# Optimization experiments

Hardware: AMD Instinct MI355X
Metric: run time of the kernel (lower is better)

The kernel has to match this reference:

```python
import jax, jax.numpy as jnp
import numpy as np

GROUPS = 8
EPS = 1e-5


def group_norm(x, gamma, beta):
    # x: (b, c, h, w); normalize per sample over each group of c//GROUPS channels and all spatial dims
    b, c, h, w = x.shape
    xg = x.reshape(b, GROUPS, c // GROUPS, h, w)
    mean = jnp.mean(xg, axis=(2, 3, 4), keepdims=True)
    var = jnp.var(xg, axis=(2, 3, 4), keepdims=True)
    xn = ((xg - mean) * jax.lax.rsqrt(var + EPS)).reshape(b, c, h, w)
    return xn * gamma[None, :, None, None] + beta[None, :, None, None]


def setup_inputs() -> dict:
    key = jax.random.key(0)
    k1, k2, k3 = jax.random.split(key, 3)
    b, c, h, w = 32, 256, 32, 32
    x = jax.random.normal(k1, (b, c, h, w), dtype=jnp.float32)
    qkv_w = jax.random.normal(k2, (3 * c, c), dtype=jnp.float32) * 0.02
    qkv_b = jnp.zeros((3 * c,), dtype=jnp.float32)
    out_w = jax.random.normal(k3, (c, c), dtype=jnp.float32) * 0.02
    out_b = jnp.zeros((c,), dtype=jnp.float32)
    gn_gamma = jnp.ones((c,), dtype=jnp.float32)
    gn_beta = jnp.zeros((c,), dtype=jnp.float32)
    return {"x": x, "gn_gamma": gn_gamma, "gn_beta": gn_beta,
            "qkv_w": qkv_w, "qkv_b": qkv_b, "out_w": out_w, "out_b": out_b}


def reference(x, gn_gamma, gn_beta, qkv_w, qkv_b, out_w, out_b):
    b, c, h, w = x.shape
    xn = group_norm(x, gn_gamma, gn_beta)
    # 1x1 conv == per-pixel linear: (b,c,h,w) x (3c,c) -> (b,3c,h,w)
    qkv = jnp.einsum('bchw,dc->bdhw', xn, qkv_w) + qkv_b[None, :, None, None]
    q, k, v = jnp.split(qkv, 3, axis=1)
    # (b, c, h, w) -> (b, hw, c)
    def tok(t):
        return t.transpose(0, 2, 3, 1).reshape(b, h * w, c)
    q, k, v = tok(q), tok(k), tok(v)
    scale = 1.0 / jnp.sqrt(jnp.asarray(c, dtype=x.dtype))
    scores = jnp.einsum('bnc,bmc->bnm', q, k) * scale  # (b, hw, hw)
    attn = jax.nn.softmax(scores, axis=-1)
    out = jnp.einsum('bnm,bmc->bnc', attn, v)  # (b, hw, c)
    out = out.reshape(b, h, w, c).transpose(0, 3, 1, 2)  # (b, c, h, w)
    out = jnp.einsum('bchw,dc->bdhw', out, out_w) + out_b[None, :, None, None]
    return out + x
```

## Files before the change

### kernel.cpp

```cpp
#include <hip/hip_runtime.h>
#include <hip/hip_bf16.h>
#include <stdint.h>


typedef __bf16 bf16_t;
typedef __bf16 bf16x4 __attribute__((ext_vector_type(4)));
typedef __bf16 bf16x8 __attribute__((ext_vector_type(8)));
typedef float f32x4 __attribute__((ext_vector_type(4)));
typedef float f32x16 __attribute__((ext_vector_type(16)));
typedef _Float16 f16x4 __attribute__((ext_vector_type(4)));

#define MFMA16(a, b, c) __builtin_amdgcn_mfma_f32_16x16x32_bf16((a), (b), (c), 0, 0, 0)
#define MFMA32(a, b, c) __builtin_amdgcn_mfma_f32_32x32x16_bf16((a), (b), (c), 0, 0, 0)
#define GLL16(g, l)                                                                     \
    __builtin_amdgcn_global_load_lds((const __attribute__((address_space(1))) void*)(g), \
                                     (__attribute__((address_space(3))) void*)(l), 16, 0, 0)

__global__ void cast_bf16(const float* __restrict__ s, bf16_t* __restrict__ d, int n) {
    for (int i = blockIdx.x * blockDim.x + threadIdx.x; i < n; i += gridDim.x * blockDim.x)
        d[i] = (bf16_t)s[i];
}

__global__ __launch_bounds__(256) void gn_kernel(const float* __restrict__ x,
                                                 const float* __restrict__ gamma,
                                                 const float* __restrict__ beta,
                                                 bf16_t* __restrict__ xn) {
    extern __shared__ char gsm[];
    float* red = (float*)(gsm + 65536);
    int bg = blockIdx.x, b = bg >> 3, g = bg & 7;
    const float* base = x + (size_t)(b * 256 + g * 32) * 1024;
    int tid = threadIdx.x;

    float s = 0.f, ss = 0.f;
    #pragma unroll 4
    for (int c = 0; c < 32; c++) {
        float4 v = *(const float4*)(base + c * 1024 + tid * 4);
        s += v.x + v.y + v.z + v.w;
        ss += v.x * v.x + v.y * v.y + v.z * v.z + v.w * v.w;
        f16x4 h = {(_Float16)v.x, (_Float16)v.y, (_Float16)v.z, (_Float16)v.w};
        *(f16x4*)(gsm + c * 2048 + ((tid * 8) ^ ((c & 7) << 4))) = h;
    }
    for (int off = 32; off; off >>= 1) { s += __shfl_down(s, off); ss += __shfl_down(ss, off); }
    if ((tid & 63) == 0) { red[tid >> 6] = s; red[4 + (tid >> 6)] = ss; }
    __syncthreads();
    float S = red[0] + red[1] + red[2] + red[3];
    float SS = red[4] + red[5] + red[6] + red[7];
    float mean = S * (1.0f / 32768.0f);
    float var = SS * (1.0f / 32768.0f) - mean * mean;
    float rstd = rsqrtf(var + 1e-5f);

    int c = tid & 31;
    float gam = gamma[g * 32 + c] * rstd;
    float bet = beta[g * 32 + c] - mean * gam;
    bf16_t* dst = xn + (size_t)(b * 1024) * 256 + g * 32 + c;
    #pragma unroll 4
    for (int it = 0; it < 128; it++) {
        int p = it * 8 + (tid >> 5);
        _Float16 hv = *(_Float16*)(gsm + c * 2048 + ((p * 2) ^ ((c & 7) << 4)));
        dst[(size_t)p * 256] = (bf16_t)((float)hv * gam + bet);
    }
}

__global__ __launch_bounds__(256) void gemm_qkv(const bf16_t* __restrict__ xn,
                                                const bf16_t* __restrict__ wq,
                                                const float* __restrict__ qkv_b,
                                                bf16_t* __restrict__ qb,
                                                bf16_t* __restrict__ kb,
                                                bf16_t* __restrict__ vt) {
    __shared__ char smem[65536];
    char* As = smem;
    char* Bs = smem + 32768;
    int tid = threadIdx.x;
    int m0 = blockIdx.x * 64, n0 = blockIdx.y * 64;
    const char* asrc = (const char*)xn + (size_t)m0 * 512;
    const char* bsrc = (const char*)wq + (size_t)n0 * 512;

    float4 ta[8], tb[8];
    #pragma unroll
    for (int i = 0; i < 8; i++) {
        int t = i * 256 + tid, row = t >> 5, sl = t & 31;
        ta[i] = *(const float4*)(asrc + row * 512 + sl * 16);
        tb[i] = *(const float4*)(bsrc + row * 512 + sl * 16);
    }
    #pragma unroll
    for (int i = 0; i < 8; i++) {
        int t = i * 256 + tid, row = t >> 5, sl = t & 31;
        int off = (sl * 16) ^ ((row & 7) << 4);
        *(float4*)(As + row * 512 + off) = ta[i];
        *(float4*)(Bs + row * 512 + off) = tb[i];
    }
    __syncthreads();

    int wv = tid >> 6, lane = tid & 63, lrow = lane & 15, lgr = lane >> 4;
    int arow = wv * 16 + lrow;
    f32x4 acc[4] = {};
    #pragma unroll
    for (int s = 0; s < 8; s++) {
        int koff = s * 64 + lgr * 16;
        bf16x8 af = *(const bf16x8*)(As + arow * 512 + (koff ^ ((arow & 7) << 4)));
        #pragma unroll
        for (int ct = 0; ct < 4; ct++) {
            int brow = ct * 16 + lrow;
            bf16x8 bfr = *(const bf16x8*)(Bs + brow * 512 + (koff ^ ((brow & 7) << 4)));
            acc[ct] = MFMA16(af, bfr, acc[ct]);
        }
    }

    if (n0 < 512) {
        #pragma unroll
        for (int ct = 0; ct < 4; ct++) {
            int d = n0 + ct * 16 + lrow;
            float bias = qkv_b[d];
            #pragma unroll
            for (int r = 0; r < 4; r++) {
                int m = m0 + wv * 16 + lgr * 4 + r;
                float val = acc[ct][r] + bias;
                if (d < 256) qb[(size_t)m * 256 + d] = (bf16_t)val;
                else kb[(size_t)m * 256 + (d - 256)] = (bf16_t)val;
            }
        }
    } else {
        __syncthreads();
        bf16_t* tt = (bf16_t*)smem;
        #pragma unroll
        for (int ct = 0; ct < 4; ct++) {
            int d = n0 + ct * 16 + lrow;
            float bias = qkv_b[d];
            #pragma unroll
            for (int r = 0; r < 4; r++)
                tt[(ct * 16 + lrow) * 66 + wv * 16 + lgr * 4 + r] = (bf16_t)(acc[ct][r] + bias);
        }
        __syncthreads();
        int bb = m0 >> 10, nbase = m0 & 1023;
        #pragma unroll
        for (int i = 0; i < 16; i++) {
            int e = i * 256 + tid;
            int d_l = e >> 6, m_l = e & 63;
            vt[(size_t)bb * 262144 + (size_t)(n0 - 512 + d_l) * 1024 + nbase + m_l] =
                tt[d_l * 66 + m_l];
        }
    }
}

__global__ __launch_bounds__(256) void attn_kernel(const bf16_t* __restrict__ qb,
                                                   const bf16_t* __restrict__ kb,
                                                   const bf16_t* __restrict__ vt,
                                                   bf16_t* __restrict__ ao) {
    extern __shared__ char smem[];
    int tid = threadIdx.x;
    int i = blockIdx.x;
    int b = (i & 7) + ((i >> 6) << 3);
    int qt = (i >> 3) & 7;
    int wv = tid >> 6, lane = tid & 63;
    int l31 = lane & 31, hi = lane >> 5;

    const char* kbase = (const char*)kb + (size_t)b * 524288;
    const char* vbase = (const char*)vt + (size_t)b * 524288;
    char* Pw = smem + 131072 + wv * 4096;

    int qg = qt * 128 + wv * 32 + l31;
    const char* qsrc = (const char*)qb + (size_t)(b * 1024 + qg) * 512;
    bf16x8 qf[16];
    #pragma unroll
    for (int ks = 0; ks < 16; ks++) qf[ks] = *(const bf16x8*)(qsrc + ks * 32 + hi * 16);

    f32x16 o[8] = {};
    float mrun = -1e30f, lrun = 0.f;

    auto stage = [&](int buf, int ch) {
        int j0 = ch * 64;
        char* Kd = smem + buf * 32768;
        char* Vd = smem + 65536 + buf * 32768;
        #pragma unroll
        for (int t = 0; t < 8; t++) {
            int r0 = wv * 16 + t * 2;
            int r = r0 + (lane >> 5), u = lane & 31;
            const char* gp = kbase + (size_t)(j0 + r) * 512 + ((u ^ (r & 7)) * 16);
            GLL16(gp, Kd + r0 * 512);
        }
        #pragma unroll
        for (int t = 0; t < 8; t++) {
            int r0 = wv * 64 + t * 8;
            int r = r0 + (lane >> 3), u = lane & 7;
            const char* gp = vbase + (size_t)r * 2048 + j0 * 2 + ((u ^ (r & 7)) * 16);
            GLL16(gp, Vd + r0 * 128);
        }
    };

    stage(0, 0);
    __syncthreads();

    for (int ch = 0; ch < 16; ch++) {
        int cur = ch & 1;
        char* Ks = smem + cur * 32768;
        char* Vs = smem + 65536 + cur * 32768;
        if (ch < 15) stage(cur ^ 1, ch + 1);

        f32x16 sc0 = {}, sc1 = {};
        #pragma unroll
        for (int ks = 0; ks < 16; ks++) {
            int col = ks * 32 + hi * 16;
            int r0 = l31, r1 = 32 + l31;
            bf16x8 k0 = *(const bf16x8*)(Ks + r0 * 512 + (col ^ ((r0 & 7) << 4)));
            bf16x8 k1 = *(const bf16x8*)(Ks + r1 * 512 + (col ^ ((r1 & 7) << 4)));
            sc0 = MFMA32(k0, qf[ks], sc0);
            sc1 = MFMA32(k1, qf[ks], sc1);
        }

        float sv0[16], sv1[16];
        float m_c = -1e30f;
        #pragma unroll
        for (int r = 0; r < 16; r++) {
            sv0[r] = sc0[r] * 0.0625f;
            sv1[r] = sc1[r] * 0.0625f;
            m_c = fmaxf(m_c, fmaxf(sv0[r], sv1[r]));
        }
        m_c = fmaxf(m_c, __shfl_xor(m_c, 32));
        float mo = mrun;
        float mn = (m_c <= mo + 8.0f) ? mo : m_c;
        float rs = 0.f;
        #pragma unroll
        for (int r = 0; r < 16; r++) {
            sv0[r] = __expf(sv0[r] - mn);
            sv1[r] = __expf(sv1[r] - mn);
            rs += sv0[r] + sv1[r];
        }
        rs += __shfl_xor(rs, 32);
        float alpha = __expf(mo - mn);
        lrun = lrun * alpha + rs;
        mrun = mn;
        #pragma unroll
        for (int rg = 0; rg < 4; rg++) {
            bf16x4 pa, pb;
            #pragma unroll
            for (int r = 0; r < 4; r++) {
                pa[r] = (bf16_t)sv0[rg * 4 + r];
                pb[r] = (bf16_t)sv1[rg * 4 + r];
            }
            int sw = (l31 & 7) << 4;
            *(bf16x4*)(Pw + l31 * 128 + ((rg * 16 + hi * 8) ^ sw)) = pa;
            *(bf16x4*)(Pw + l31 * 128 + ((64 + rg * 16 + hi * 8) ^ sw)) = pb;
        }
        if (__any(mn != mo)) {
            #pragma unroll
            for (int dt = 0; dt < 8; dt++) o[dt] = o[dt] * alpha;
        }

        #pragma unroll
        for (int ks = 0; ks < 4; ks++) {
            int pcol = (ks * 32 + hi * 16) ^ ((l31 & 7) << 4);
            bf16x8 pf = *(const bf16x8*)(Pw + l31 * 128 + pcol);
            #pragma unroll
            for (int dt = 0; dt < 8; dt++) {
                int d = dt * 32 + l31;
                bf16x8 vf =
                    *(const bf16x8*)(Vs + d * 128 + ((ks * 32 + hi * 16) ^ ((d & 7) << 4)));
                o[dt] = MFMA32(vf, pf, o[dt]);
            }
        }
        __syncthreads();
    }

    float inv = 1.0f / lrun;
    char* aod = (char*)ao + (size_t)(b * 1024 + qg) * 512;
    #pragma unroll
    for (int dt = 0; dt < 8; dt++) {
        #pragma unroll
        for (int rg = 0; rg < 4; rg++) {
            bf16x4 w;
            #pragma unroll
            for (int r = 0; r < 4; r++) w[r] = (bf16_t)(o[dt][rg * 4 + r] * inv);
            *(bf16x4*)(aod + dt * 64 + rg * 16 + hi * 8) = w;
        }
    }
}

__global__ __launch_bounds__(256) void gemm_out(const bf16_t* __restrict__ wo,
                                                const bf16_t* __restrict__ ao,
                                                const float* __restrict__ out_b,
                                                const float* __restrict__ x,
                                                float* __restrict__ out) {
    __shared__ char smem[65536];
    char* As = smem;
    char* Bs = smem + 32768;
    int tid = threadIdx.x;
    int c0 = blockIdx.x * 64, n0 = blockIdx.y * 64, b = blockIdx.z;
    const char* asrc = (const char*)wo + (size_t)c0 * 512;
    const char* bsrc = (const char*)ao + ((size_t)b * 1024 + n0) * 512;

    float4 ta[8], tb[8];
    #pragma unroll
    for (int i = 0; i < 8; i++) {
        int t = i * 256 + tid, row = t >> 5, sl = t & 31;
        ta[i] = *(const float4*)(asrc + row * 512 + sl * 16);
        tb[i] = *(const float4*)(bsrc + row * 512 + sl * 16);
    }
    #pragma unroll
    for (int i = 0; i < 8; i++) {
        int t = i * 256 + tid, row = t >> 5, sl = t & 31;
        int off = (sl * 16) ^ ((row & 7) << 4);
        *(float4*)(As + row * 512 + off) = ta[i];
        *(float4*)(Bs + row * 512 + off) = tb[i];
    }
    __syncthreads();

    int wv = tid >> 6, lane = tid & 63, lrow = lane & 15, lgr = lane >> 4;
    int arow = wv * 16 + lrow;
    f32x4 acc[4] = {};
    #pragma unroll
    for (int s = 0; s < 8; s++) {
        int koff = s * 64 + lgr * 16;
        bf16x8 af = *(const bf16x8*)(As + arow * 512 + (koff ^ ((arow & 7) << 4)));
        #pragma unroll
        for (int ct = 0; ct < 4; ct++) {
            int brow = ct * 16 + lrow;
            bf16x8 bfr = *(const bf16x8*)(Bs + brow * 512 + (koff ^ ((brow & 7) << 4)));
            acc[ct] = MFMA16(af, bfr, acc[ct]);
        }
    }

    #pragma unroll
    for (int ct = 0; ct < 4; ct++) {
        int n = n0 + ct * 16 + lrow;
        #pragma unroll
        for (int r = 0; r < 4; r++) {
            int c = c0 + wv * 16 + lgr * 4 + r;
            size_t idx = ((size_t)b * 256 + c) * 1024 + n;
            out[idx] = acc[ct][r] + out_b[c] + x[idx];
        }
    }
}

extern "C" void kernel_launch(void* const* d_in, const int* in_sizes, int n_in,
                              void* d_out, int out_size, void* d_ws, size_t ws_size,
                              hipStream_t stream) {
    (void)in_sizes; (void)n_in; (void)out_size; (void)ws_size;
    const float* x      = (const float*)d_in[0];
    const float* gamma  = (const float*)d_in[1];
    const float* beta   = (const float*)d_in[2];
    const float* qkv_w  = (const float*)d_in[3];
    const float* qkv_b  = (const float*)d_in[4];
    const float* out_w  = (const float*)d_in[5];
    const float* out_b  = (const float*)d_in[6];
    float* out = (float*)d_out;

    char* ws = (char*)d_ws;
    const size_t MB16 = 16777216;
    bf16_t* xn  = (bf16_t*)(ws);
    bf16_t* qb  = (bf16_t*)(ws + 1 * MB16);
    bf16_t* kb  = (bf16_t*)(ws + 2 * MB16);
    bf16_t* vt  = (bf16_t*)(ws + 3 * MB16);
    bf16_t* ao  = (bf16_t*)(ws + 4 * MB16);
    bf16_t* wqb = (bf16_t*)(ws + 5 * MB16);
    bf16_t* wob = (bf16_t*)(ws + 5 * MB16 + 393216);

    cast_bf16<<<192, 256, 0, stream>>>(qkv_w, wqb, 196608);
    cast_bf16<<<64, 256, 0, stream>>>(out_w, wob, 65536);
    gn_kernel<<<256, 256, 65600, stream>>>(x, gamma, beta, xn);
    gemm_qkv<<<dim3(512, 12), 256, 0, stream>>>(xn, wqb, qkv_b, qb, kb, vt);
    attn_kernel<<<256, 256, 147456, stream>>>(qb, kb, vt, ao);
    gemm_out<<<dim3(4, 16, 32), 256, 0, stream>>>(wob, ao, out_b, x, out);
}
```

Baseline: 144.0 us.

## Rewrite GEMMs with 128x128 tiles and software-pipeline attention loop

The QKV projection is split into a Q/K GEMM and a separate V GEMM that writes V transposed directly. All GEMMs move to 128x128 tiles staged with direct global-to-LDS loads and 32x32 MFMA, which cuts per-block overhead and increases operand reuse. The attention kernel now pipelines QK^T of the next chunk against softmax and PV of the previous one, using split K/V staging with explicit waitcnt barriers. It folds the softmax scale (with log2e) into Q so it can use exp2f, and builds the P fragments in registers with permlane32 swaps instead of a round trip through LDS. The cost is higher register pressure, larger LDS use and more delicate synchronization.

```diff
diff --git a/kernel.cpp b/kernel.cpp
--- a/kernel.cpp
+++ b/kernel.cpp
@@ -10,11 +10,23 @@
 typedef float f32x16 __attribute__((ext_vector_type(16)));
 typedef _Float16 f16x4 __attribute__((ext_vector_type(4)));
 
-#define MFMA16(a, b, c) __builtin_amdgcn_mfma_f32_16x16x32_bf16((a), (b), (c), 0, 0, 0)
 #define MFMA32(a, b, c) __builtin_amdgcn_mfma_f32_32x32x16_bf16((a), (b), (c), 0, 0, 0)
 #define GLL16(g, l)                                                                     \
     __builtin_amdgcn_global_load_lds((const __attribute__((address_space(1))) void*)(g), \
                                      (__attribute__((address_space(3))) void*)(l), 16, 0, 0)
+#define WAITV8 asm volatile("s_waitcnt vmcnt(8)" ::: "memory")
+#define WAITV0 asm volatile("s_waitcnt vmcnt(0)" ::: "memory")
+#define WLG0   asm volatile("s_waitcnt lgkmcnt(0)" ::: "memory")
+#define SBAR   __builtin_amdgcn_s_barrier()
+#define SCH0   __builtin_amdgcn_sched_barrier(0)
+
+#define QSCALE 0.0901684400555f
+
+__device__ inline uint32_t pack2(float a, float b) {
+    union { uint32_t u; __bf16 h[2]; } w;
+    w.h[0] = (__bf16)a; w.h[1] = (__bf16)b;
+    return w.u;
+}
 
 __global__ void cast_bf16(const float* __restrict__ s, bf16_t* __restrict__ d, int n) {
     for (int i = blockIdx.x * blockDim.x + threadIdx.x; i < n; i += gridDim.x * blockDim.x)
@@ -61,218 +73,103 @@
     }
 }
 
-__global__ __launch_bounds__(256) void gemm_qkv(const bf16_t* __restrict__ xn,
-                                                const bf16_t* __restrict__ wq,
-                                                const float* __restrict__ qkv_b,
-                                                bf16_t* __restrict__ qb,
-                                                bf16_t* __restrict__ kb,
-                                                bf16_t* __restrict__ vt) {
-    __shared__ char smem[65536];
-    char* As = smem;
-    char* Bs = smem + 32768;
-    int tid = threadIdx.x;
-    int m0 = blockIdx.x * 64, n0 = blockIdx.y * 64;
-    const char* asrc = (const char*)xn + (size_t)m0 * 512;
-    const char* bsrc = (const char*)wq + (size_t)n0 * 512;
-
-    float4 ta[8], tb[8];
-    #pragma unroll
-    for (int i = 0; i < 8; i++) {
-        int t = i * 256 + tid, row = t >> 5, sl = t & 31;
-        ta[i] = *(const float4*)(asrc + row * 512 + sl * 16);
-        tb[i] = *(const float4*)(bsrc + row * 512 + sl * 16);
-    }
-    #pragma unroll
-    for (int i = 0; i < 8; i++) {
-        int t = i * 256 + tid, row = t >> 5, sl = t & 31;
-        int off = (sl * 16) ^ ((row & 7) << 4);
-        *(float4*)(As + row * 512 + off) = ta[i];
-        *(float4*)(Bs + row * 512 + off) = tb[i];
-    }
+__device__ inline void stage128(const char* src, char* dstLDS, int wv, int lane) {
+    int r2 = lane >> 5, u = lane & 31;
+    #pragma unroll
+    for (int t = 0; t < 16; t++) {
+        int row = t * 8 + wv * 2 + r2;
+        GLL16(src + (size_t)row * 512 + ((u ^ (row & 7)) * 16), dstLDS + (t * 8 + wv * 2) * 512);
+    }
+}
+__device__ inline bf16x8 lds_frag(const char* base, int row, int sl) {
+    return *(const bf16x8*)(base + row * 512 + ((sl ^ (row & 7)) * 16));
+}
+
+__global__ __launch_bounds__(256) void gemm_qk(const bf16_t* __restrict__ xn,
+                                               const bf16_t* __restrict__ wq,
+                                               const float* __restrict__ qkv_b,
+                                               bf16_t* __restrict__ qb,
+                                               bf16_t* __restrict__ kb) {
+    extern __shared__ char smem[];
+    char* As = smem; char* Bs = smem + 65536;
+    int tid = threadIdx.x, wv = tid >> 6, lane = tid & 63;
+    int m0 = blockIdx.x * 128, n0 = blockIdx.y * 128;
+    stage128((const char*)xn + (size_t)m0 * 512, As, wv, lane);
+    stage128((const char*)wq + (size_t)n0 * 512, Bs, wv, lane);
     __syncthreads();
 
-    int wv = tid >> 6, lane = tid & 63, lrow = lane & 15, lgr = lane >> 4;
-    int arow = wv * 16 + lrow;
-    f32x4 acc[4] = {};
-    #pragma unroll
-    for (int s = 0; s < 8; s++) {
-        int koff = s * 64 + lgr * 16;
-        bf16x8 af = *(const bf16x8*)(As + arow * 512 + (koff ^ ((arow & 7) << 4)));
-        #pragma unroll
-        for (int ct = 0; ct < 4; ct++) {
-            int brow = ct * 16 + lrow;
-            bf16x8 bfr = *(const bf16x8*)(Bs + brow * 512 + (koff ^ ((brow & 7) << 4)));
-            acc[ct] = MFMA16(af, bfr, acc[ct]);
-        }
-    }
-
-    if (n0 < 512) {
-        #pragma unroll
-        for (int ct = 0; ct < 4; ct++) {
-            int d = n0 + ct * 16 + lrow;
-            float bias = qkv_b[d];
-            #pragma unroll
-            for (int r = 0; r < 4; r++) {
-                int m = m0 + wv * 16 + lgr * 4 + r;
-                float val = acc[ct][r] + bias;
-                if (d < 256) qb[(size_t)m * 256 + d] = (bf16_t)val;
-                else kb[(size_t)m * 256 + (d - 256)] = (bf16_t)val;
+    int wr = wv >> 1, wc = wv & 1, l31 = lane & 31, hi = lane >> 5;
+    f32x16 acc[2][2] = {};
+    #pragma unroll
+    for (int ks = 0; ks < 16; ks++) {
+        int sl = ks * 2 + hi;
+        bf16x8 a0 = lds_frag(As, wr * 64 + l31, sl);
+        bf16x8 a1 = lds_frag(As, wr * 64 + 32 + l31, sl);
+        bf16x8 b0 = lds_frag(Bs, wc * 64 + l31, sl);
+        bf16x8 b1 = lds_frag(Bs, wc * 64 + 32 + l31, sl);
+        acc[0][0] = MFMA32(a0, b0, acc[0][0]);
+        acc[0][1] = MFMA32(a0, b1, acc[0][1]);
+        acc[1][0] = MFMA32(a1, b0, acc[1][0]);
+        acc[1][1] = MFMA32(a1, b1, acc[1][1]);
+    }
+    #pragma unroll
+    for (int ms = 0; ms < 2; ms++)
+        #pragma unroll
+        for (int ns = 0; ns < 2; ns++) {
+            int n = n0 + wc * 64 + ns * 32 + l31;
+            float bias = qkv_b[n];
+            bool isq = n < 256;
+            float sc = isq ? QSCALE : 1.0f;
+            bf16_t* dst = isq ? qb : kb;
+            int d = isq ? n : n - 256;
+            #pragma unroll
+            for (int r = 0; r < 16; r++) {
+                int m = m0 + wr * 64 + ms * 32 + (r & 3) + 8 * (r >> 2) + 4 * hi;
+                dst[(size_t)m * 256 + d] = (bf16_t)((acc[ms][ns][r] + bias) * sc);
             }
         }
-    } else {
-        __syncthreads();
-        bf16_t* tt = (bf16_t*)smem;
-        #pragma unroll
-        for (int ct = 0; ct < 4; ct++) {
-            int d = n0 + ct * 16 + lrow;
-            float bias = qkv_b[d];
-            #pragma unroll
-            for (int r = 0; r < 4; r++)
-                tt[(ct * 16 + lrow) * 66 + wv * 16 + lgr * 4 + r] = (bf16_t)(acc[ct][r] + bias);
-        }
-        __syncthreads();
-        int bb = m0 >> 10, nbase = m0 & 1023;
-        #pragma unroll
-        for (int i = 0; i < 16; i++) {
-            int e = i * 256 + tid;
-            int d_l = e >> 6, m_l = e & 63;
-            vt[(size_t)bb * 262144 + (size_t)(n0 - 512 + d_l) * 1024 + nbase + m_l] =
-                tt[d_l * 66 + m_l];
-        }
-    }
-}
-
-__global__ __launch_bounds__(256) void attn_kernel(const bf16_t* __restrict__ qb,
-                                                   const bf16_t* __restrict__ kb,
-                                                   const bf16_t* __restrict__ vt,
-                                                   bf16_t* __restrict__ ao) {
+}
+
+__global__ __launch_bounds__(256) void gemm_v(const bf16_t* __restrict__ xn,
+                                              const bf16_t* __restrict__ wq,
+                                              const float* __restrict__ qkv_b,
+                                              bf16_t* __restrict__ vt) {
     extern __shared__ char smem[];
-    int tid = threadIdx.x;
-    int i = blockIdx.x;
-    int b = (i & 7) + ((i >> 6) << 3);
-    int qt = (i >> 3) & 7;
-    int wv = tid >> 6, lane = tid & 63;
-    int l31 = lane & 31, hi = lane >> 5;
-
-    const char* kbase = (const char*)kb + (size_t)b * 524288;
-    const char* vbase = (const char*)vt + (size_t)b * 524288;
-    char* Pw = smem + 131072 + wv * 4096;
-
-    int qg = qt * 128 + wv * 32 + l31;
-    const char* qsrc = (const char*)qb + (size_t)(b * 1024 + qg) * 512;
-    bf16x8 qf[16];
-    #pragma unroll
-    for (int ks = 0; ks < 16; ks++) qf[ks] = *(const bf16x8*)(qsrc + ks * 32 + hi * 16);
-
-    f32x16 o[8] = {};
-    float mrun = -1e30f, lrun = 0.f;
-
-    auto stage = [&](int buf, int ch) {
-        int j0 = ch * 64;
-        char* Kd = smem + buf * 32768;
-        char* Vd = smem + 65536 + buf * 32768;
-        #pragma unroll
-        for (int t = 0; t < 8; t++) {
-            int r0 = wv * 16 + t * 2;
-            int r = r0 + (lane >> 5), u = lane & 31;
-            const char* gp = kbase + (size_t)(j0 + r) * 512 + ((u ^ (r & 7)) * 16);
-            GLL16(gp, Kd + r0 * 512);
-        }
-        #pragma unroll
-        for (int t = 0; t < 8; t++) {
-            int r0 = wv * 64 + t * 8;
-            int r = r0 + (lane >> 3), u = lane & 7;
-            const char* gp = vbase + (size_t)r * 2048 + j0 * 2 + ((u ^ (r & 7)) * 16);
-            GLL16(gp, Vd + r0 * 128);
-        }
-    };
-
-    stage(0, 0);
+    char* As = smem; char* Bs = smem + 65536;
+    int tid = threadIdx.x, wv = tid >> 6, lane = tid & 63;
+    int d0 = blockIdx.x * 128, t0 = blockIdx.y * 128;
+    stage128((const char*)wq + (size_t)(512 + d0) * 512, As, wv, lane);
+    stage128((const char*)xn + (size_t)t0 * 512, Bs, wv, lane);
     __syncthreads();
 
-    for (int ch = 0; ch < 16; ch++) {
-        int cur = ch & 1;
-        char* Ks = smem + cur * 32768;
-        char* Vs = smem + 65536 + cur * 32768;
-        if (ch < 15) stage(cur ^ 1, ch + 1);
-
-        f32x16 sc0 = {}, sc1 = {};
-        #pragma unroll
-        for (int ks = 0; ks < 16; ks++) {
-            int col = ks * 32 + hi * 16;
-            int r0 = l31, r1 = 32 + l31;
-            bf16x8 k0 = *(const bf16x8*)(Ks + r0 * 512 + (col ^ ((r0 & 7) << 4)));
-            bf16x8 k1 = *(const bf16x8*)(Ks + r1 * 512 + (col ^ ((r1 & 7) << 4)));
-            sc0 = MFMA32(k0, qf[ks], sc0);
-            sc1 = MFMA32(k1, qf[ks], sc1);
-        }
-
-        float sv0[16], sv1[16];
-        float m_c = -1e30f;
-        #pragma unroll
-        for (int r = 0; r < 16; r++) {
-            sv0[r] = sc0[r] * 0.0625f;
-            sv1[r] = sc1[r] * 0.0625f;
-            m_c = fmaxf(m_c, fmaxf(sv0[r], sv1[r]));
-        }
-        m_c = fmaxf(m_c, __shfl_xor(m_c, 32));
-        float mo = mrun;
-        float mn = (m_c <= mo + 8.0f) ? mo : m_c;
-        float rs = 0.f;
-        #pragma unroll
-        for (int r = 0; r < 16; r++) {
-            sv0[r] = __expf(sv0[r] - mn);
-            sv1[r] = __expf(sv1[r] - mn);
-            rs += sv0[r] + sv1[r];
-        }
-        rs += __shfl_xor(rs, 32);
-        float alpha = __expf(mo - mn);
-        lrun = lrun * alpha + rs;
-        mrun = mn;
-        #pragma unroll
-        for (int rg = 0; rg < 4; rg++) {
-            bf16x4 pa, pb;
-            #pragma unroll
-            for (int r = 0; r < 4; r++) {
-                pa[r] = (bf16_t)sv0[rg * 4 + r];
-                pb[r] = (bf16_t)sv1[rg * 4 + r];
+    int wr = wv >> 1, wc = wv & 1, l31 = lane & 31, hi = lane >> 5;
+    f32x16 acc[2][2] = {};
+    #pragma unroll
+    for (int ks = 0; ks < 16; ks++) {
+        int sl = ks * 2 + hi;
+        bf16x8 a0 = lds_frag(As, wr * 64 + l31, sl);
+        bf16x8 a1 = lds_frag(As, wr * 64 + 32 + l31, sl);
+        bf16x8 b0 = lds_frag(Bs, wc * 64 + l31, sl);
+        bf16x8 b1 = lds_frag(Bs, wc * 64 + 32 + l31, sl);
+        acc[0][0] = MFMA32(a0, b0, acc[0][0]);
+        acc[0][1] = MFMA32(a0, b1, acc[0][1]);
+        acc[1][0] = MFMA32(a1, b0, acc[1][0]);
+        acc[1][1] = MFMA32(a1, b1, acc[1][1]);
+    }
+    #pragma unroll
+    for (int ms = 0; ms < 2; ms++)
+        #pragma unroll
+        for (int ns = 0; ns < 2; ns++) {
+            int tok0 = t0 + wc * 64 + ns * 32;
+            #pragma unroll
+            for (int r = 0; r < 16; r++) {
+                int d = d0 + wr * 64 + ms * 32 + (r & 3) + 8 * (r >> 2) + 4 * hi;
+                int tok = tok0 + l31;
+                int bb = tok >> 10, pos = tok & 1023;
+                vt[(size_t)bb * 262144 + (size_t)d * 1024 + pos] =
+                    (bf16_t)(acc[ms][ns][r] + qkv_b[512 + d]);
             }
-            int sw = (l31 & 7) << 4;
-            *(bf16x4*)(Pw + l31 * 128 + ((rg * 16 + hi * 8) ^ sw)) = pa;
-            *(bf16x4*)(Pw + l31 * 128 + ((64 + rg * 16 + hi * 8) ^ sw)) = pb;
-        }
-        if (__any(mn != mo)) {
-            #pragma unroll
-            for (int dt = 0; dt < 8; dt++) o[dt] = o[dt] * alpha;
-        }
-
-        #pragma unroll
-        for (int ks = 0; ks < 4; ks++) {
-            int pcol = (ks * 32 + hi * 16) ^ ((l31 & 7) << 4);
-            bf16x8 pf = *(const bf16x8*)(Pw + l31 * 128 + pcol);
-            #pragma unroll
-            for (int dt = 0; dt < 8; dt++) {
-                int d = dt * 32 + l31;
-                bf16x8 vf =
-                    *(const bf16x8*)(Vs + d * 128 + ((ks * 32 + hi * 16) ^ ((d & 7) << 4)));
-                o[dt] = MFMA32(vf, pf, o[dt]);
-            }
-        }
-        __syncthreads();
-    }
-
-    float inv = 1.0f / lrun;
-    char* aod = (char*)ao + (size_t)(b * 1024 + qg) * 512;
-    #pragma unroll
-    for (int dt = 0; dt < 8; dt++) {
-        #pragma unroll
-        for (int rg = 0; rg < 4; rg++) {
-            bf16x4 w;
-            #pragma unroll
-            for (int r = 0; r < 4; r++) w[r] = (bf16_t)(o[dt][rg * 4 + r] * inv);
-            *(bf16x4*)(aod + dt * 64 + rg * 16 + hi * 8) = w;
-        }
-    }
+        }
 }
 
 __global__ __launch_bounds__(256) void gemm_out(const bf16_t* __restrict__ wo,
@@ -280,53 +177,176 @@
                                                 const float* __restrict__ out_b,
                                                 const float* __restrict__ x,
                                                 float* __restrict__ out) {
-    __shared__ char smem[65536];
-    char* As = smem;
-    char* Bs = smem + 32768;
-    int tid = threadIdx.x;
-    int c0 = blockIdx.x * 64, n0 = blockIdx.y * 64, b = blockIdx.z;
-    const char* asrc = (const char*)wo + (size_t)c0 * 512;
-    const char* bsrc = (const char*)ao + ((size_t)b * 1024 + n0) * 512;
-
-    float4 ta[8], tb[8];
-    #pragma unroll
-    for (int i = 0; i < 8; i++) {
-        int t = i * 256 + tid, row = t >> 5, sl = t & 31;
-        ta[i] = *(const float4*)(asrc + row * 512 + sl * 16);
-        tb[i] = *(const float4*)(bsrc + row * 512 + sl * 16);
-    }
-    #pragma unroll
-    for (int i = 0; i < 8; i++) {
-        int t = i * 256 + tid, row = t >> 5, sl = t & 31;
-        int off = (sl * 16) ^ ((row & 7) << 4);
-        *(float4*)(As + row * 512 + off) = ta[i];
-        *(float4*)(Bs + row * 512 + off) = tb[i];
-    }
+    extern __shared__ char smem[];
+    char* As = smem; char* Bs = smem + 65536;
+    int tid = threadIdx.x, wv = tid >> 6, lane = tid & 63;
+    int c0 = blockIdx.x * 128, t0 = blockIdx.y * 128;
+    stage128((const char*)wo + (size_t)c0 * 512, As, wv, lane);
+    stage128((const char*)ao + (size_t)t0 * 512, Bs, wv, lane);
     __syncthreads();
 
-    int wv = tid >> 6, lane = tid & 63, lrow = lane & 15, lgr = lane >> 4;
-    int arow = wv * 16 + lrow;
-    f32x4 acc[4] = {};
-    #pragma unroll
-    for (int s = 0; s < 8; s++) {
-        int koff = s * 64 + lgr * 16;
-        bf16x8 af = *(const bf16x8*)(As + arow * 512 + (koff ^ ((arow & 7) << 4)));
-        #pragma unroll
-        for (int ct = 0; ct < 4; ct++) {
-            int brow = ct * 16 + lrow;
-            bf16x8 bfr = *(const bf16x8*)(Bs + brow * 512 + (koff ^ ((brow & 7) << 4)));
-            acc[ct] = MFMA16(af, bfr, acc[ct]);
-        }
-    }
-
-    #pragma unroll
-    for (int ct = 0; ct < 4; ct++) {
-        int n = n0 + ct * 16 + lrow;
-        #pragma unroll
-        for (int r = 0; r < 4; r++) {
-            int c = c0 + wv * 16 + lgr * 4 + r;
-            size_t idx = ((size_t)b * 256 + c) * 1024 + n;
-            out[idx] = acc[ct][r] + out_b[c] + x[idx];
+    int wr = wv >> 1, wc = wv & 1, l31 = lane & 31, hi = lane >> 5;
+    f32x16 acc[2][2] = {};
+    #pragma unroll
+    for (int ks = 0; ks < 16; ks++) {
+        int sl = ks * 2 + hi;
+        bf16x8 a0 = lds_frag(As, wr * 64 + l31, sl);
+        bf16x8 a1 = lds_frag(As, wr * 64 + 32 + l31, sl);
+        bf16x8 b0 = lds_frag(Bs, wc * 64 + l31, sl);
+        bf16x8 b1 = lds_frag(Bs, wc * 64 + 32 + l31, sl);
+        acc[0][0] = MFMA32(a0, b0, acc[0][0]);
+        acc[0][1] = MFMA32(a0, b1, acc[0][1]);
+        acc[1][0] = MFMA32(a1, b0, acc[1][0]);
+        acc[1][1] = MFMA32(a1, b1, acc[1][1]);
+    }
+    #pragma unroll
+    for (int ms = 0; ms < 2; ms++)
+        #pragma unroll
+        for (int ns = 0; ns < 2; ns++) {
+            #pragma unroll
+            for (int r = 0; r < 16; r++) {
+                int c = c0 + wr * 64 + ms * 32 + (r & 3) + 8 * (r >> 2) + 4 * hi;
+                int tok = t0 + wc * 64 + ns * 32 + l31;
+                int bb = tok >> 10, pos = tok & 1023;
+                size_t idx = ((size_t)bb * 256 + c) * 1024 + pos;
+                out[idx] = acc[ms][ns][r] + out_b[c] + x[idx];
+            }
+        }
+}
+
+__global__ __launch_bounds__(256, 1) void attn_kernel(const bf16_t* __restrict__ qb,
+                                                      const bf16_t* __restrict__ kb,
+                                                      const bf16_t* __restrict__ vt,
+                                                      bf16_t* __restrict__ ao) {
+    extern __shared__ char smem[];
+    int tid = threadIdx.x, i = blockIdx.x;
+    int b = (i & 7) + ((i >> 6) << 3);
+    int qt = (i >> 3) & 7;
+    int wv = tid >> 6, lane = tid & 63, l31 = lane & 31, hi = lane >> 5;
+
+    const char* kbase = (const char*)kb + (size_t)b * 524288;
+    const char* vbase = (const char*)vt + (size_t)b * 524288;
+
+    int qg = qt * 128 + wv * 32 + l31;
+    const char* qsrc = (const char*)qb + (size_t)(b * 1024 + qg) * 512;
+    bf16x8 qf[16];
+    #pragma unroll
+    for (int ks = 0; ks < 16; ks++) qf[ks] = *(const bf16x8*)(qsrc + ks * 32 + hi * 16);
+
+    f32x16 o[8] = {};
+    f32x16 sp0 = {}, sp1 = {};
+    float mrun = -1e30f, lrun = 0.f;
+
+    auto stage_K = [&](int ch) {
+        char* Kd = smem + (ch & 1) * 32768;
+        int j0 = ch * 64;
+        #pragma unroll
+        for (int t = 0; t < 8; t++) {
+            int r0 = wv * 16 + t * 2;
+            int r = r0 + (lane >> 5), u = lane & 31;
+            GLL16(kbase + (size_t)(j0 + r) * 512 + ((u ^ (r & 7)) * 16), Kd + r0 * 512);
+        }
+    };
+    auto stage_V = [&](int ch) {
+        char* Vd = smem + 65536 + (ch & 1) * 32768;
+        int j0 = ch * 64;
+        #pragma unroll
+        for (int t = 0; t < 8; t++) {
+            int r0 = wv * 64 + t * 8;
+            int r = r0 + (lane >> 3), u = lane & 7;
+            GLL16(vbase + (size_t)r * 2048 + j0 * 2 + ((u ^ (r & 7)) * 16), Vd + r0 * 128);
+        }
+    };
+    auto qkt = [&](int ch, f32x16& s0, f32x16& s1) {
+        const char* Ks = smem + (ch & 1) * 32768;
+        #pragma unroll
+        for (int ks = 0; ks < 16; ks++) {
+            int col = ks * 32 + hi * 16;
+            bf16x8 k0 = *(const bf16x8*)(Ks + l31 * 512 + (col ^ ((l31 & 7) << 4)));
+            bf16x8 k1 = *(const bf16x8*)(Ks + (32 + l31) * 512 + (col ^ ((l31 & 7) << 4)));
+            s0 = MFMA32(k0, qf[ks], s0);
+            s1 = MFMA32(k1, qf[ks], s1);
+        }
+    };
+    auto smax_pv = [&](int ch) {
+        float mc = -1e30f;
+        #pragma unroll
+        for (int r = 0; r < 16; r++) mc = fmaxf(mc, fmaxf(sp0[r], sp1[r]));
+        mc = fmaxf(mc, __shfl_xor(mc, 32));
+        float mo = mrun;
+        float mn = (mc <= mo + 8.0f) ? mo : mc;
+        float rs = 0.f;
+        #pragma unroll
+        for (int r = 0; r < 16; r++) {
+            sp0[r] = exp2f(sp0[r] - mn);
+            sp1[r] = exp2f(sp1[r] - mn);
+            rs += sp0[r] + sp1[r];
+        }
+        rs += __shfl_xor(rs, 32);
+        float al = exp2f(mo - mn);
+        lrun = lrun * al + rs;
+        mrun = mn;
+        if (__any(mn != mo)) {
+            #pragma unroll
+            for (int dt = 0; dt < 8; dt++) o[dt] = o[dt] * al;
+        }
+        const char* Vs = smem + 65536 + (ch & 1) * 32768;
+        #pragma unroll
+        for (int pk = 0; pk < 4; pk++) {
+            float e0 = (pk < 2) ? sp0[(pk & 1) * 8 + 0] : sp1[(pk & 1) * 8 + 0];
+            float e1 = (pk < 2) ? sp0[(pk & 1) * 8 + 1] : sp1[(pk & 1) * 8 + 1];
+            float e2 = (pk < 2) ? sp0[(pk & 1) * 8 + 2] : sp1[(pk & 1) * 8 + 2];
+            float e3 = (pk < 2) ? sp0[(pk & 1) * 8 + 3] : sp1[(pk & 1) * 8 + 3];
+            float e4 = (pk < 2) ? sp0[(pk & 1) * 8 + 4] : sp1[(pk & 1) * 8 + 4];
+            float e5 = (pk < 2) ? sp0[(pk & 1) * 8 + 5] : sp1[(pk & 1) * 8 + 5];
+            float e6 = (pk < 2) ? sp0[(pk & 1) * 8 + 6] : sp1[(pk & 1) * 8 + 6];
+            float e7 = (pk < 2) ? sp0[(pk & 1) * 8 + 7] : sp1[(pk & 1) * 8 + 7];
+            uint32_t A0 = pack2(e0, e1), A1 = pack2(e2, e3);
+            uint32_t B0 = pack2(e4, e5), B1 = pack2(e6, e7);
+            asm volatile("v_permlane32_swap_b32 %0, %1" : "+v"(B0), "+v"(A0));
+            asm volatile("v_permlane32_swap_b32 %0, %1" : "+v"(B1), "+v"(A1));
+            union { bf16x8 v; uint32_t u[4]; } pw;
+            pw.u[0] = A0; pw.u[1] = A1; pw.u[2] = B0; pw.u[3] = B1;
+            #pragma unroll
+            for (int dt = 0; dt < 8; dt++) {
+                int d = dt * 32 + l31;
+                bf16x8 vf =
+                    *(const bf16x8*)(Vs + d * 128 + ((pk * 32 + hi * 16) ^ ((d & 7) << 4)));
+                o[dt] = MFMA32(vf, pw.v, o[dt]);
+            }
+        }
+    };
+
+    stage_K(0); stage_V(0);
+    WAITV8; SCH0; SBAR;
+    stage_K(1);
+    qkt(0, sp0, sp1);
+    WLG0; SCH0; SBAR;
+    stage_V(1);
+
+    for (int ch = 1; ch < 16; ch++) {
+        WAITV8; SCH0; SBAR;
+        if (ch < 15) stage_K(ch + 1);
+        f32x16 sn0 = {}, sn1 = {};
+        qkt(ch, sn0, sn1);
+        smax_pv(ch - 1);
+        WLG0; SCH0; SBAR;
+        if (ch < 15) stage_V(ch + 1);
+        sp0 = sn0; sp1 = sn1;
+    }
+    WAITV0; SCH0; SBAR;
+    smax_pv(15);
+
+    float inv = 1.0f / lrun;
+    char* aod = (char*)ao + (size_t)(b * 1024 + qg) * 512;
+    #pragma unroll
+    for (int dt = 0; dt < 8; dt++) {
+        #pragma unroll
+        for (int rg = 0; rg < 4; rg++) {
+            bf16x4 w;
+            #pragma unroll
+            for (int r = 0; r < 4; r++) w[r] = (bf16_t)(o[dt][rg * 4 + r] * inv);
+            *(bf16x4*)(aod + dt * 64 + rg * 16 + hi * 8) = w;
         }
     }
 }
@@ -357,7 +377,8 @@
     cast_bf16<<<192, 256, 0, stream>>>(qkv_w, wqb, 196608);
     cast_bf16<<<64, 256, 0, stream>>>(out_w, wob, 65536);
     gn_kernel<<<256, 256, 65600, stream>>>(x, gamma, beta, xn);
-    gemm_qkv<<<dim3(512, 12), 256, 0, stream>>>(xn, wqb, qkv_b, qb, kb, vt);
-    attn_kernel<<<256, 256, 147456, stream>>>(qb, kb, vt, ao);
-    gemm_out<<<dim3(4, 16, 32), 256, 0, stream>>>(wob, ao, out_b, x, out);
-}
+    gemm_qk<<<dim3(256, 4), 256, 131072, stream>>>(xn, wqb, qkv_b, qb, kb);
+    gemm_v<<<dim3(2, 256), 256, 131072, stream>>>(xn, wqb, qkv_b, vt);
+    attn_kernel<<<256, 256, 131072, stream>>>(qb, kb, vt, ao);
+    gemm_out<<<dim3(2, 256), 256, 131072, stream>>>(wob, ao, out_b, x, out);
+}
```

Result: no change. 142.5 us (-1.1%).
